# Performance work log

Hardware: AMD Instinct MI355X
Metric: run time of the kernel (lower is better)

## Reference

```python
import jax, jax.numpy as jnp
import numpy as np

B, S, D = 2, 2048, 512
H = 8
G = 4
LAMBDA_INIT = 0.2  # 0.8 - 0.6*exp(-0.3*(layer_idx-1)) with layer_idx=1
EPS = 1e-5


def setup_inputs() -> dict:
    key = jax.random.key(0)
    ks = jax.random.split(key, 16)
    n = jax.random.normal
    return {
        "x": n(ks[0], (B, S, D), jnp.float32),
        "K1_w": n(ks[1], (D, D), jnp.float32) * 0.02,
        "K1_b": n(ks[2], (D,), jnp.float32) * 0.02,
        "Q1_w": n(ks[3], (D, D), jnp.float32) * 0.02,
        "K2_w": n(ks[4], (D, D), jnp.float32) * 0.02,
        "K2_b": n(ks[5], (D,), jnp.float32) * 0.02,
        "Q2_w": n(ks[6], (D, D), jnp.float32) * 0.02,
        "V_w": n(ks[7], (D, D), jnp.float32) * 0.02,
        "lambda_q1": n(ks[8], (H, 1), jnp.float32),
        "lambda_k1": n(ks[9], (H, 1), jnp.float32),
        "lambda_q2": n(ks[10], (H, 1), jnp.float32),
        "lambda_k2": n(ks[11], (H, 1), jnp.float32),
        "gn_w": jnp.ones((D,), jnp.float32),
        "gn_b": jnp.zeros((D,), jnp.float32),
        "out_w": n(ks[12], (D, D), jnp.float32) * 0.02,
        "out_b": n(ks[13], (D,), jnp.float32) * 0.02,
    }


def reference(x, K1_w, K1_b, Q1_w, K2_w, K2_b, Q2_w, V_w,
              lambda_q1, lambda_k1, lambda_q2, lambda_k2,
              gn_w, gn_b, out_w, out_b):
    b, s, d = x.shape
    hd = d // H

    def heads(t):  # (b,s,d) -> (b,H,s,hd)
        return t.reshape(b, s, H, hd).transpose(0, 2, 1, 3)

    q1 = heads(x @ Q1_w.T)
    k1 = heads(x @ K1_w.T + K1_b)
    q2 = heads(x @ Q2_w.T)
    k2 = heads(x @ K2_w.T + K2_b)
    v = heads(x @ V_w.T)

    scale = hd ** 0.5
    a1 = jax.nn.softmax(jnp.einsum('bhqd,bhkd->bhqk', q1, k1) / scale, axis=-1)
    a2 = jax.nn.softmax(jnp.einsum('bhqd,bhkd->bhqk', q2, k2) / scale, axis=-1)

    lam = (jnp.exp(lambda_q1 * lambda_k1)
           - jnp.exp(lambda_q2 * lambda_k2) + LAMBDA_INIT)  # (H,1)
    attn = a1 - lam.reshape(1, H, 1, 1) * a2

    o = jnp.einsum('bhqk,bhkd->bhqd', attn, v)
    o = o.transpose(0, 2, 1, 3).reshape(b, s, d)

    # GroupNorm over channels: input (b, d, s), groups G normalize over (d/G, s)
    xc = o.transpose(0, 2, 1).reshape(b, G, d // G, s)
    mu = xc.mean(axis=(2, 3), keepdims=True)
    var = xc.var(axis=(2, 3), keepdims=True)
    xn = ((xc - mu) * jax.lax.rsqrt(var + EPS)).reshape(b, d, s)
    xn = xn * gn_w[None, :, None] + gn_b[None, :, None]

    y = xn.transpose(0, 2, 1) @ out_w.T + out_b
    return y
```

## Files before the change

kernel.cpp:

```cpp
#include <hip/hip_runtime.h>
#include <hip/hip_bf16.h>

typedef __bf16 bf16;
typedef __attribute__((ext_vector_type(8))) __bf16 bf16x8;
typedef __attribute__((ext_vector_type(4))) float f32x4;

#define MFMA16(a, b, c) __builtin_amdgcn_mfma_f32_16x16x32_bf16((a), (b), (c), 0, 0, 0)

static constexpr float EPS = 1e-5f;
static constexpr float LAMBDA_INIT = 0.2f;

__device__ __forceinline__ bf16x8 cvt8(const float* p) {
    const f32x4 a = *(const f32x4*)p;
    const f32x4 b = *(const f32x4*)(p + 4);
    bf16x8 r;
    r[0] = (bf16)a[0]; r[1] = (bf16)a[1]; r[2] = (bf16)a[2]; r[3] = (bf16)a[3];
    r[4] = (bf16)b[0]; r[5] = (bf16)b[1]; r[6] = (bf16)b[2]; r[7] = (bf16)b[3];
    return r;
}

__device__ __forceinline__ void gload_lds16(const void* g, void* l) {
    __builtin_amdgcn_global_load_lds(
        (const __attribute__((address_space(1))) unsigned int*)g,
        (__attribute__((address_space(3))) unsigned int*)l,
        16, 0, 0);
}

__global__ __launch_bounds__(256) void proj_kernel(
    const float* __restrict__ x,
    const float* __restrict__ q1w, const float* __restrict__ k1w,
    const float* __restrict__ q2w, const float* __restrict__ k2w,
    const float* __restrict__ vw,
    const float* __restrict__ k1b, const float* __restrict__ k2b,
    bf16* __restrict__ q1o, bf16* __restrict__ k1o,
    bf16* __restrict__ q2o, bf16* __restrict__ k2o,
    bf16* __restrict__ vto)
{
    __shared__ __align__(16) float As[128 * 32];
    __shared__ __align__(16) float Bs[128 * 32];

    const int tid = threadIdx.x;
    const int wave = tid >> 6, lane = tid & 63;
    const int l15 = lane & 15, quad = lane >> 4;
    const int wm = wave >> 1, wn = wave & 1;

    const int mb = blockIdx.x / 20;
    const int nb = blockIdx.x % 20;
    const int wsel = nb >> 2;
    const int nrow0 = (nb & 3) * 128;

    const float* W = (wsel == 0) ? q1w : (wsel == 1) ? k1w :
                     (wsel == 2) ? q2w : (wsel == 3) ? k2w : vw;

    const int srow = lane >> 3;
    const int scol = (lane & 7) * 4;
    const float* xg = x + (size_t)(mb * 128 + srow) * 512 + scol;
    const float* wg = W + (size_t)(nrow0 + srow) * 512 + scol;

    f32x4 acc[4][4];
#pragma unroll
    for (int i = 0; i < 4; ++i)
#pragma unroll
        for (int j = 0; j < 4; ++j)
            acc[i][j] = (f32x4){0.f, 0.f, 0.f, 0.f};

    for (int k0 = 0; k0 < 512; k0 += 32) {
#pragma unroll
        for (int c = 0; c < 4; ++c) {
            const int chunk = wave * 4 + c;
            gload_lds16(xg + (size_t)(chunk * 8) * 512 + k0, As + chunk * 256);
            gload_lds16(wg + (size_t)(chunk * 8) * 512 + k0, Bs + chunk * 256);
        }
        __syncthreads();

        bf16x8 af[4], bfr[4];
#pragma unroll
        for (int i = 0; i < 4; ++i)
            af[i] = cvt8(As + (wm * 64 + i * 16 + l15) * 32 + quad * 8);
#pragma unroll
        for (int j = 0; j < 4; ++j)
            bfr[j] = cvt8(Bs + (wn * 64 + j * 16 + l15) * 32 + quad * 8);

#pragma unroll
        for (int i = 0; i < 4; ++i)
#pragma unroll
            for (int j = 0; j < 4; ++j)
                acc[i][j] = MFMA16(af[i], bfr[j], acc[i][j]);

        __syncthreads();
    }

    const float scale = (wsel == 0 || wsel == 2) ? 0.125f : 1.0f;
#pragma unroll
    for (int j = 0; j < 4; ++j) {
        const int ncol = nrow0 + wn * 64 + j * 16 + l15;
        float bias = 0.f;
        if (wsel == 1) bias = k1b[ncol];
        if (wsel == 3) bias = k2b[ncol];
        const int h = ncol >> 6, hd = ncol & 63;
#pragma unroll
        for (int i = 0; i < 4; ++i) {
#pragma unroll
            for (int r = 0; r < 4; ++r) {
                const int m = mb * 128 + wm * 64 + i * 16 + quad * 4 + r;
                const int bidx = m >> 11, s = m & 2047;
                const float v = acc[i][j][r] * scale + bias;
                if (wsel == 4) {
                    const int s5 = s & 31;
                    const int p = ((s5 & 15) >> 2) * 8 + (s5 & 3) + ((s5 >> 4) << 2);
                    const int sp = (s & ~31) | p;
                    vto[((size_t)(bidx * 8 + h) * 64 + hd) * 2048 + sp] = (bf16)v;
                } else {
                    bf16* dst = (wsel == 0) ? q1o : (wsel == 1) ? k1o :
                                (wsel == 2) ? q2o : k2o;
                    dst[((size_t)(bidx * 8 + h) * 2048 + s) * 64 + hd] = (bf16)v;
                }
            }
        }
    }
}

__global__ __launch_bounds__(512, 4) void attn_kernel(
    const bf16* __restrict__ q1, const bf16* __restrict__ k1,
    const bf16* __restrict__ q2, const bf16* __restrict__ k2,
    const bf16* __restrict__ vt,
    const float* __restrict__ lq1, const float* __restrict__ lk1,
    const float* __restrict__ lq2, const float* __restrict__ lk2,
    bf16* __restrict__ o, float* __restrict__ stats)
{
    __shared__ __align__(16) bf16 smem[12288];
    __shared__ float lbuf[8][2][16];
    __shared__ float sred[8][2];

    const int tid = threadIdx.x;
    const int wave = tid >> 6;
    const int lane = tid & 63;
    const int l15 = lane & 15, quad = lane >> 4;
    const int qtile = wave & 3;
    const int kg = wave >> 2;

    const int bh = blockIdx.x >> 5;
    const int qt = blockIdx.x & 31;
    const int b = bh >> 3, h = bh & 7;

    const bf16* k1t = k1 + (size_t)bh * 2048 * 64;
    const bf16* k2t = k2 + (size_t)bh * 2048 * 64;
    const bf16* vtt = vt + (size_t)bh * 64 * 2048;

    const int qrow = qt * 64 + qtile * 16 + l15;
    const bf16* q1p = q1 + ((size_t)bh * 2048 + qrow) * 64 + quad * 8;
    const bf16* q2p = q2 + ((size_t)bh * 2048 + qrow) * 64 + quad * 8;
    const bf16x8 q1f0 = *(const bf16x8*)(q1p);
    const bf16x8 q1f1 = *(const bf16x8*)(q1p + 32);
    const bf16x8 q2f0 = *(const bf16x8*)(q2p);
    const bf16x8 q2f1 = *(const bf16x8*)(q2p + 32);

    const int sw = wave & 3;
    const int skey0 = (wave < 4) ? 0 : 1024;
    bf16* k1dst = smem + wave * 512;
    bf16* k2dst = smem + 4096 + wave * 512;
    bf16* vdst  = smem + 8192 + wave * 512;
    const size_t ksrc0 = (size_t)(skey0 + sw * 8 + (lane >> 3)) * 64
                       + 8 * ((lane & 7) ^ (lane >> 3));
    const size_t vsrc0 = (size_t)(sw * 16 + (lane >> 2)) * 2048 + skey0 + (lane & 3) * 8;

    const bf16* k1r = smem + kg * 2048;
    const bf16* k2r = smem + 4096 + kg * 2048;
    const bf16* vr  = smem + 8192 + kg * 2048;

    const int koffa = 8 * (quad ^ (l15 & 7));
    const int koffb = 8 * ((quad + 4) ^ (l15 & 7));

    f32x4 O1[4], O2[4];
    float l1 = 0.f, l2 = 0.f;
#pragma unroll
    for (int t = 0; t < 4; ++t) {
        O1[t] = (f32x4){0.f, 0.f, 0.f, 0.f};
        O2[t] = (f32x4){0.f, 0.f, 0.f, 0.f};
    }

    for (int it = 0; it < 32; ++it) {
        const size_t koff = ksrc0 + (size_t)it * 32 * 64;
        gload_lds16(k1t + koff, k1dst);
        gload_lds16(k2t + koff, k2dst);
        gload_lds16(vtt + vsrc0 + it * 32, vdst);
        __syncthreads();

        const bf16x8 k1t0a = *(const bf16x8*)(k1r + l15 * 64 + koffa);
        const bf16x8 k1t0b = *(const bf16x8*)(k1r + l15 * 64 + koffb);
        const bf16x8 k1t1a = *(const bf16x8*)(k1r + (16 + l15) * 64 + koffa);
        const bf16x8 k1t1b = *(const bf16x8*)(k1r + (16 + l15) * 64 + koffb);
        const bf16x8 k2t0a = *(const bf16x8*)(k2r + l15 * 64 + koffa);
        const bf16x8 k2t0b = *(const bf16x8*)(k2r + l15 * 64 + koffb);
        const bf16x8 k2t1a = *(const bf16x8*)(k2r + (16 + l15) * 64 + koffa);
        const bf16x8 k2t1b = *(const bf16x8*)(k2r + (16 + l15) * 64 + koffb);
        const bf16x8 v0 = *(const bf16x8*)(vr + l15 * 32 + quad * 8);
        const bf16x8 v1 = *(const bf16x8*)(vr + (16 + l15) * 32 + quad * 8);
        const bf16x8 v2 = *(const bf16x8*)(vr + (32 + l15) * 32 + quad * 8);
        const bf16x8 v3 = *(const bf16x8*)(vr + (48 + l15) * 32 + quad * 8);

        f32x4 z = (f32x4){0.f, 0.f, 0.f, 0.f};
        f32x4 s1t0 = MFMA16(k1t0a, q1f0, z);  s1t0 = MFMA16(k1t0b, q1f1, s1t0);
        f32x4 s1t1 = MFMA16(k1t1a, q1f0, z);  s1t1 = MFMA16(k1t1b, q1f1, s1t1);
        f32x4 s2t0 = MFMA16(k2t0a, q2f0, z);  s2t0 = MFMA16(k2t0b, q2f1, s2t0);
        f32x4 s2t1 = MFMA16(k2t1a, q2f0, z);  s2t1 = MFMA16(k2t1b, q2f1, s2t1);

        bf16x8 b1, b2;
#pragma unroll
        for (int r = 0; r < 4; ++r) {
            float e;
            e = __expf(s1t0[r]); l1 += e; b1[r]     = (bf16)e;
            e = __expf(s1t1[r]); l1 += e; b1[4 + r] = (bf16)e;
            e = __expf(s2t0[r]); l2 += e; b2[r]     = (bf16)e;
            e = __expf(s2t1[r]); l2 += e; b2[4 + r] = (bf16)e;
        }

        O1[0] = MFMA16(v0, b1, O1[0]);
        O1[1] = MFMA16(v1, b1, O1[1]);
        O1[2] = MFMA16(v2, b1, O1[2]);
        O1[3] = MFMA16(v3, b1, O1[3]);
        O2[0] = MFMA16(v0, b2, O2[0]);
        O2[1] = MFMA16(v1, b2, O2[1]);
        O2[2] = MFMA16(v2, b2, O2[2]);
        O2[3] = MFMA16(v3, b2, O2[3]);

        __syncthreads();
    }

    l1 += __shfl_xor(l1, 16, 64);  l1 += __shfl_xor(l1, 32, 64);
    l2 += __shfl_xor(l2, 16, 64);  l2 += __shfl_xor(l2, 32, 64);
    if (lane < 16) {
        lbuf[wave][0][lane] = l1;
        lbuf[wave][1][lane] = l2;
    }
    __syncthreads();

    f32x4* rb = (f32x4*)smem;
    if (wave == 4 || wave == 5) {
        f32x4* dst = rb + (wave - 4) * 512;
#pragma unroll
        for (int t = 0; t < 4; ++t) {
            dst[t * 64 + lane]       = O1[t];
            dst[(4 + t) * 64 + lane] = O2[t];
        }
    }
    __syncthreads();
    if (wave == 0 || wave == 1) {
        const f32x4* src = rb + wave * 512;
#pragma unroll
        for (int t = 0; t < 4; ++t) {
            O1[t] += src[t * 64 + lane];
            O2[t] += src[(4 + t) * 64 + lane];
        }
    }
    __syncthreads();
    if (wave == 6 || wave == 7) {
        f32x4* dst = rb + (wave - 6) * 512;
#pragma unroll
        for (int t = 0; t < 4; ++t) {
            dst[t * 64 + lane]       = O1[t];
            dst[(4 + t) * 64 + lane] = O2[t];
        }
    }
    __syncthreads();
    if (wave == 2 || wave == 3) {
        const f32x4* src = rb + (wave - 2) * 512;
#pragma unroll
        for (int t = 0; t < 4; ++t) {
            O1[t] += src[t * 64 + lane];
            O2[t] += src[(4 + t) * 64 + lane];
        }
    }

    float ssum = 0.f, ssq = 0.f;
    if (wave < 4) {
        const float L1 = l1 + lbuf[wave + 4][0][l15];
        const float L2 = l2 + lbuf[wave + 4][1][l15];
        const float lam = __expf(lq1[h] * lk1[h]) - __expf(lq2[h] * lk2[h]) + LAMBDA_INIT;
        const float inv1 = 1.f / L1;
        const float inv2 = lam / L2;
        const size_t row = (size_t)(b * 2048 + qt * 64 + wave * 16 + l15) * 512 + h * 64;
#pragma unroll
        for (int t = 0; t < 4; ++t) {
#pragma unroll
            for (int r = 0; r < 4; ++r) {
                const float val = O1[t][r] * inv1 - O2[t][r] * inv2;
                ssum += val;
                ssq += val * val;
                o[row + t * 16 + quad * 4 + r] = (bf16)val;
            }
        }
    }
#pragma unroll
    for (int off = 1; off < 64; off <<= 1) {
        ssum += __shfl_xor(ssum, off, 64);
        ssq += __shfl_xor(ssq, off, 64);
    }
    if (lane == 0) { sred[wave][0] = ssum; sred[wave][1] = ssq; }
    __syncthreads();
    if (tid == 0) {
        float s0 = 0.f, s1 = 0.f;
        for (int w = 0; w < 8; ++w) { s0 += sred[w][0]; s1 += sred[w][1]; }
        const int bg = b * 4 + (h >> 1);
        atomicAdd(&stats[bg * 2], s0);
        atomicAdd(&stats[bg * 2 + 1], s1);
    }
}

__global__ __launch_bounds__(256) void out_gemm_kernel(
    const bf16* __restrict__ o, const float* __restrict__ stats,
    const float* __restrict__ gnw, const float* __restrict__ gnb,
    const float* __restrict__ ow, const float* __restrict__ ob,
    float* __restrict__ y)
{
    const int lane = threadIdx.x & 63;
    const int wave = threadIdx.x >> 6;
    const int l15 = lane & 15, quad = lane >> 4;

    const int tile = blockIdx.x * 4 + wave;
    const int mt = tile >> 4;
    const int nt = tile & 15;
    const int b = mt >> 5;

    const float N = 128.f * 2048.f;
    float mu[4], rs[4];
#pragma unroll
    for (int g = 0; g < 4; ++g) {
        const float m = stats[(b * 4 + g) * 2] / N;
        const float var = stats[(b * 4 + g) * 2 + 1] / N - m * m;
        mu[g] = m;
        rs[g] = rsqrtf(var + EPS);
    }

    const bf16* ap[4];
#pragma unroll
    for (int i = 0; i < 4; ++i)
        ap[i] = o + (size_t)(mt * 64 + i * 16 + l15) * 512 + quad * 8;
    const float* bp[2];
#pragma unroll
    for (int j = 0; j < 2; ++j)
        bp[j] = ow + (size_t)(nt * 32 + j * 16 + l15) * 512 + quad * 8;

    f32x4 acc[4][2];
#pragma unroll
    for (int i = 0; i < 4; ++i)
#pragma unroll
        for (int j = 0; j < 2; ++j)
            acc[i][j] = (f32x4){0.f, 0.f, 0.f, 0.f};

    for (int kk = 0; kk < 16; ++kk) {
        const int g = kk >> 2;
        const int c0 = kk * 32 + quad * 8;
        const f32x4 w0 = *(const f32x4*)(gnw + c0);
        const f32x4 w1 = *(const f32x4*)(gnw + c0 + 4);
        const f32x4 g0 = *(const f32x4*)(gnb + c0);
        const f32x4 g1 = *(const f32x4*)(gnb + c0 + 4);
        float weff[8], beff[8];
#pragma unroll
        for (int j = 0; j < 4; ++j) {
            weff[j] = w0[j] * rs[g];  beff[j] = g0[j] - mu[g] * weff[j];
            weff[4 + j] = w1[j] * rs[g];  beff[4 + j] = g1[j] - mu[g] * weff[4 + j];
        }

        bf16x8 af[4], bfr[2];
#pragma unroll
        for (int i = 0; i < 4; ++i) {
            const bf16x8 ov = *(const bf16x8*)(ap[i] + kk * 32);
#pragma unroll
            for (int j = 0; j < 8; ++j)
                af[i][j] = (bf16)((float)ov[j] * weff[j] + beff[j]);
        }
#pragma unroll
        for (int j = 0; j < 2; ++j) bfr[j] = cvt8(bp[j] + kk * 32);
#pragma unroll
        for (int i = 0; i < 4; ++i)
#pragma unroll
            for (int j = 0; j < 2; ++j)
                acc[i][j] = MFMA16(af[i], bfr[j], acc[i][j]);
    }

#pragma unroll
    for (int j = 0; j < 2; ++j) {
        const int ncol = nt * 32 + j * 16 + l15;
        const float bias = ob[ncol];
#pragma unroll
        for (int i = 0; i < 4; ++i) {
#pragma unroll
            for (int r = 0; r < 4; ++r) {
                const int m = mt * 64 + i * 16 + quad * 4 + r;
                y[(size_t)m * 512 + ncol] = acc[i][j][r] + bias;
            }
        }
    }
}

extern "C" void kernel_launch(void* const* d_in, const int* in_sizes, int n_in,
                              void* d_out, int out_size, void* d_ws, size_t ws_size,
                              hipStream_t stream)
{
    const float* x   = (const float*)d_in[0];
    const float* K1w = (const float*)d_in[1];
    const float* K1b = (const float*)d_in[2];
    const float* Q1w = (const float*)d_in[3];
    const float* K2w = (const float*)d_in[4];
    const float* K2b = (const float*)d_in[5];
    const float* Q2w = (const float*)d_in[6];
    const float* Vw  = (const float*)d_in[7];
    const float* lq1 = (const float*)d_in[8];
    const float* lk1 = (const float*)d_in[9];
    const float* lq2 = (const float*)d_in[10];
    const float* lk2 = (const float*)d_in[11];
    const float* gnw = (const float*)d_in[12];
    const float* gnb = (const float*)d_in[13];
    const float* Ow  = (const float*)d_in[14];
    const float* Ob  = (const float*)d_in[15];

    const size_t SZ = (size_t)2 * 8 * 2048 * 64;
    bf16* q1 = (bf16*)d_ws;
    bf16* k1 = q1 + SZ;
    bf16* q2 = k1 + SZ;
    bf16* k2 = q2 + SZ;
    bf16* vt = k2 + SZ;
    bf16* o  = vt + SZ;
    float* stats = (float*)(o + SZ);

    hipMemsetAsync(stats, 0, 16 * sizeof(float), stream);

    proj_kernel<<<640, 256, 0, stream>>>(x, Q1w, K1w, Q2w, K2w, Vw, K1b, K2b,
                                         q1, k1, q2, k2, vt);
    attn_kernel<<<512, 512, 0, stream>>>(q1, k1, q2, k2, vt,
                                         lq1, lk1, lq2, lk2, o, stats);
    out_gemm_kernel<<<256, 256, 0, stream>>>(o, stats, gnw, gnb, Ow, Ob,
                                             (float*)d_out);
}
```

Before: 202.4 us.

## Fold GroupNorm affine into pre-scaled output weights and stage GEMM tiles in LDS

```diff
diff --git a/kernel.cpp b/kernel.cpp
--- a/kernel.cpp
+++ b/kernel.cpp
@@ -307,20 +307,50 @@
     }
 }
 
+__global__ __launch_bounds__(256) void prep_kernel(
+    const float* __restrict__ ow, const float* __restrict__ gnw,
+    const float* __restrict__ gnb, bf16* __restrict__ owg,
+    float* __restrict__ S0)
+{
+    __shared__ float red[4];
+    const int tid = threadIdx.x;
+    const int n0 = blockIdx.x * 16;
+    const int c0 = tid, c1 = tid + 256;
+
+    const float gw0 = gnw[c0], gw1 = gnw[c1];
+    const float gb0 = gnb[c0], gb1 = gnb[c1];
+
+    for (int n = 0; n < 16; ++n) {
+        const size_t rowb = (size_t)(n0 + n) * 512;
+        const float w0 = ow[rowb + c0];
+        const float w1 = ow[rowb + c1];
+        owg[rowb + c0] = (bf16)(w0 * gw0);
+        owg[rowb + c1] = (bf16)(w1 * gw1);
+        float s = gb0 * w0 + gb1 * w1;
+#pragma unroll
+        for (int off = 1; off < 64; off <<= 1) s += __shfl_xor(s, off, 64);
+        if ((tid & 63) == 0) red[tid >> 6] = s;
+        __syncthreads();
+        if (tid == 0) S0[n0 + n] = red[0] + red[1] + red[2] + red[3];
+        __syncthreads();
+    }
+}
+
 __global__ __launch_bounds__(256) void out_gemm_kernel(
-    const bf16* __restrict__ o, const float* __restrict__ stats,
-    const float* __restrict__ gnw, const float* __restrict__ gnb,
-    const float* __restrict__ ow, const float* __restrict__ ob,
-    float* __restrict__ y)
+    const bf16* __restrict__ o, const bf16* __restrict__ owg,
+    const float* __restrict__ S0, const float* __restrict__ stats,
+    const float* __restrict__ ob, float* __restrict__ y)
 {
-    const int lane = threadIdx.x & 63;
-    const int wave = threadIdx.x >> 6;
+    __shared__ __align__(16) bf16 As[64 * 32];
+    __shared__ __align__(16) bf16 Bs[64 * 32];
+
+    const int tid = threadIdx.x;
+    const int wave = tid >> 6, lane = tid & 63;
     const int l15 = lane & 15, quad = lane >> 4;
 
-    const int tile = blockIdx.x * 4 + wave;
-    const int mt = tile >> 4;
-    const int nt = tile & 15;
-    const int b = mt >> 5;
+    const int mb = blockIdx.x >> 3;
+    const int nb = blockIdx.x & 7;
+    const int b = mb >> 5;
 
     const float N = 128.f * 2048.f;
     float mu[4], rs[4];
@@ -332,64 +362,70 @@
         rs[g] = rsqrtf(var + EPS);
     }
 
-    const bf16* ap[4];
-#pragma unroll
-    for (int i = 0; i < 4; ++i)
-        ap[i] = o + (size_t)(mt * 64 + i * 16 + l15) * 512 + quad * 8;
-    const float* bp[2];
-#pragma unroll
-    for (int j = 0; j < 2; ++j)
-        bp[j] = ow + (size_t)(nt * 32 + j * 16 + l15) * 512 + quad * 8;
-
-    f32x4 acc[4][2];
-#pragma unroll
-    for (int i = 0; i < 4; ++i)
-#pragma unroll
-        for (int j = 0; j < 2; ++j)
-            acc[i][j] = (f32x4){0.f, 0.f, 0.f, 0.f};
+    const int srow = wave * 16 + (lane >> 2);
+    const int scol = (lane & 3) * 8;
+    const bf16* ag = o + (size_t)(mb * 64 + srow) * 512 + scol;
+    const bf16* bg = owg + (size_t)(nb * 64 + srow) * 512 + scol;
+    bf16* adst = As + wave * 512;
+    bf16* bdst = Bs + wave * 512;
+
+    f32x4 acc[4], tot[4];
+#pragma unroll
+    for (int i = 0; i < 4; ++i) {
+        acc[i] = (f32x4){0.f, 0.f, 0.f, 0.f};
+        tot[i] = (f32x4){0.f, 0.f, 0.f, 0.f};
+    }
+    float s1g[4];
+    float s1p = 0.f;
+#pragma unroll
+    for (int g = 0; g < 4; ++g) s1g[g] = 0.f;
 
     for (int kk = 0; kk < 16; ++kk) {
-        const int g = kk >> 2;
-        const int c0 = kk * 32 + quad * 8;
-        const f32x4 w0 = *(const f32x4*)(gnw + c0);
-        const f32x4 w1 = *(const f32x4*)(gnw + c0 + 4);
-        const f32x4 g0 = *(const f32x4*)(gnb + c0);
-        const f32x4 g1 = *(const f32x4*)(gnb + c0 + 4);
-        float weff[8], beff[8];
-#pragma unroll
-        for (int j = 0; j < 4; ++j) {
-            weff[j] = w0[j] * rs[g];  beff[j] = g0[j] - mu[g] * weff[j];
-            weff[4 + j] = w1[j] * rs[g];  beff[4 + j] = g1[j] - mu[g] * weff[4 + j];
-        }
-
-        bf16x8 af[4], bfr[2];
-#pragma unroll
-        for (int i = 0; i < 4; ++i) {
-            const bf16x8 ov = *(const bf16x8*)(ap[i] + kk * 32);
-#pragma unroll
-            for (int j = 0; j < 8; ++j)
-                af[i][j] = (bf16)((float)ov[j] * weff[j] + beff[j]);
-        }
-#pragma unroll
-        for (int j = 0; j < 2; ++j) bfr[j] = cvt8(bp[j] + kk * 32);
+        gload_lds16(ag + kk * 32, adst);
+        gload_lds16(bg + kk * 32, bdst);
+        __syncthreads();
+
+        bf16x8 af[4];
 #pragma unroll
         for (int i = 0; i < 4; ++i)
-#pragma unroll
-            for (int j = 0; j < 2; ++j)
-                acc[i][j] = MFMA16(af[i], bfr[j], acc[i][j]);
-    }
-
-#pragma unroll
-    for (int j = 0; j < 2; ++j) {
-        const int ncol = nt * 32 + j * 16 + l15;
-        const float bias = ob[ncol];
-#pragma unroll
-        for (int i = 0; i < 4; ++i) {
-#pragma unroll
-            for (int r = 0; r < 4; ++r) {
-                const int m = mt * 64 + i * 16 + quad * 4 + r;
-                y[(size_t)m * 512 + ncol] = acc[i][j][r] + bias;
+            af[i] = *(const bf16x8*)(As + (i * 16 + l15) * 32 + quad * 8);
+        const bf16x8 bf = *(const bf16x8*)(Bs + (wave * 16 + l15) * 32 + quad * 8);
+
+#pragma unroll
+        for (int i = 0; i < 4; ++i)
+            acc[i] = MFMA16(af[i], bf, acc[i]);
+
+#pragma unroll
+        for (int j = 0; j < 8; ++j) s1p += (float)bf[j];
+
+        __syncthreads();
+
+        if ((kk & 3) == 3) {
+            const int g = kk >> 2;
+#pragma unroll
+            for (int i = 0; i < 4; ++i) {
+#pragma unroll
+                for (int r = 0; r < 4; ++r) tot[i][r] += rs[g] * acc[i][r];
+                acc[i] = (f32x4){0.f, 0.f, 0.f, 0.f};
             }
+            float sg = s1p + __shfl_xor(s1p, 16, 64);
+            sg += __shfl_xor(sg, 32, 64);
+            s1g[g] = sg;
+            s1p = 0.f;
+        }
+    }
+
+    const int ncol = nb * 64 + wave * 16 + l15;
+    float bias = S0[ncol] + ob[ncol];
+#pragma unroll
+    for (int g = 0; g < 4; ++g) bias -= mu[g] * rs[g] * s1g[g];
+
+#pragma unroll
+    for (int i = 0; i < 4; ++i) {
+#pragma unroll
+        for (int r = 0; r < 4; ++r) {
+            const int m = mb * 64 + i * 16 + quad * 4 + r;
+            y[(size_t)m * 512 + ncol] = tot[i][r] + bias;
         }
     }
 }
@@ -422,14 +458,17 @@
     bf16* k2 = q2 + SZ;
     bf16* vt = k2 + SZ;
     bf16* o  = vt + SZ;
-    float* stats = (float*)(o + SZ);
+    bf16* owg = o + SZ;
+    float* S0 = (float*)(owg + 512 * 512);
+    float* stats = S0 + 512;
 
     hipMemsetAsync(stats, 0, 16 * sizeof(float), stream);
 
     proj_kernel<<<640, 256, 0, stream>>>(x, Q1w, K1w, Q2w, K2w, Vw, K1b, K2b,
                                          q1, k1, q2, k2, vt);
+    prep_kernel<<<32, 256, 0, stream>>>(Ow, gnw, gnb, owg, S0);
     attn_kernel<<<512, 512, 0, stream>>>(q1, k1, q2, k2, vt,
                                          lq1, lk1, lq2, lk2, o, stats);
-    out_gemm_kernel<<<256, 256, 0, stream>>>(o, stats, gnw, gnb, Ow, Ob,
+    out_gemm_kernel<<<512, 256, 0, stream>>>(o, owg, S0, stats, Ob,
                                              (float*)d_out);
 }
```

Measured after the change: 200.4 us. Within noise of the previous version (-1.0%).
